# Performance work log

Hardware: AMD Instinct MI355X
Metric: run time of the kernel (lower is better)

Reference implementation:

```python
import jax, jax.numpy as jnp
import numpy as np

NUM_HEADS = 8
EPS = 1e-12  # torch F.normalize eps


def _l2norm(t):
    n = jnp.linalg.norm(t, axis=-1, keepdims=True)
    return t / jnp.maximum(n, EPS)


def setup_inputs() -> dict:
    key = jax.random.key(0)
    k1, k2, k3 = jax.random.split(key, 3)
    B, T, N, D = 16, 12, 1024, 128
    x = jax.random.normal(k1, (B, T, N, D), dtype=jnp.float32)
    # Linear(model_dim, 3*model_dim, bias=False): stored as (D, 3D) for x @ W
    W_qkv = jax.random.normal(k2, (D, 3 * D), dtype=jnp.float32) * (1.0 / np.sqrt(D))
    W_out = jax.random.normal(k3, (D, D), dtype=jnp.float32) * (1.0 / np.sqrt(D))
    b_out = jnp.zeros((D,), dtype=jnp.float32)
    return {"x": x, "W_qkv": W_qkv, "W_out": W_out, "b_out": b_out}


def reference(x, W_qkv, W_out, b_out):
    B, T, N, D = x.shape
    H = NUM_HEADS
    hd = D // H
    qkv = x @ W_qkv                                  # (B,T,N,3D)
    q, k, v = jnp.split(qkv, 3, axis=-1)
    # split heads + flatten (B,T) -> b = B*T, matching torch stack/flatten
    qs = _l2norm(q.reshape(B * T, N, H, hd))          # (b,N,H,m)
    ks = _l2norm(k.reshape(B * T, N, H, hd))
    vs = v.reshape(B * T, N, H, hd)
    # linear attention: running kv sum + normalizer
    kvs = jnp.einsum('blhm,blhd->bhmd', ks, vs)       # (b,H,m,d)
    attn_num = jnp.einsum('bnhm,bhmd->bnhd', qs, kvs) + N * vs
    ks_sum = jnp.sum(ks, axis=1)                      # (b,H,m)
    normalizer = jnp.einsum('bnhm,bhm->bnh', qs, ks_sum)[..., None] + N
    out = attn_num / normalizer                       # (b,N,H,d)
    out = out.reshape(B, T, N, D)
    return out @ W_out + b_out
```

## Files before the change

### kernel.cpp

```cpp
#include <hip/hip_runtime.h>

#define NBATCH 192
#define SEQ    1024
#define DIM    128
#define NH     8
#define EPS    1e-12f

typedef short bf16x8 __attribute__((ext_vector_type(8)));
typedef float f32x4  __attribute__((ext_vector_type(4)));

#define KVS_F  393216
#define ZERO_F 417792

static __device__ __forceinline__ unsigned short f2bf(float f) {
    unsigned u = __builtin_bit_cast(unsigned, f);
    u += 0x7fff + ((u >> 16) & 1);
    return (unsigned short)(u >> 16);
}

template <int CTRL>
static __device__ __forceinline__ float dpp_add(float v) {
    int j = __builtin_amdgcn_mov_dpp(__builtin_bit_cast(int, v), CTRL, 0xf, 0xf, false);
    return v + __builtin_bit_cast(float, j);
}
static __device__ __forceinline__ float r16sum(float v) {
    v = dpp_add<0xB1>(v);
    v = dpp_add<0x4E>(v);
    v = dpp_add<0x141>(v);
    v = dpp_add<0x140>(v);
    return v;
}

static __device__ __forceinline__ int strip_addr(int row, int el) {
    return row * 32 + ((((el >> 3) ^ (row & 3)) << 3) | (el & 7));
}

static __device__ __forceinline__ uint2 pack4(float a, float b, float c, float d) {
    uint2 r;
    r.x = (unsigned)f2bf(a) | ((unsigned)f2bf(b) << 16);
    r.y = (unsigned)f2bf(c) | ((unsigned)f2bf(d) << 16);
    return r;
}

static __device__ __forceinline__ bf16x8 cvt8(float4 a, float4 b) {
    bf16x8 r;
    r[0] = (short)f2bf(a.x); r[1] = (short)f2bf(a.y); r[2] = (short)f2bf(a.z); r[3] = (short)f2bf(a.w);
    r[4] = (short)f2bf(b.x); r[5] = (short)f2bf(b.y); r[6] = (short)f2bf(b.z); r[7] = (short)f2bf(b.w);
    return r;
}

static __device__ __forceinline__ bf16x8 gfrag(const unsigned short* __restrict__ wT,
                                               int ct, int ks, int lane) {
    return *reinterpret_cast<const bf16x8*>(wT + ((ct * 4 + ks) * 64 + lane) * 8);
}

__global__ __launch_bounds__(256) void k0_prep(const float* __restrict__ Wqkv,
                                               const float* __restrict__ Wout,
                                               unsigned short* __restrict__ wsWT) {
    int i = blockIdx.x * 256 + threadIdx.x;
    int which = i >> 14, e = i & 16383;
    int j = e & 7, f = e >> 3;
    int n15 = f & 15, q = (f >> 4) & 3, ks = (f >> 6) & 3, ct = f >> 8;
    int k = ks * 32 + q * 8 + j, n = ct * 16 + n15;
    float v = (which < 3) ? Wqkv[k * 384 + which * 128 + n] : Wout[k * 128 + n];
    wsWT[i] = f2bf(v);
}

__global__ __launch_bounds__(512, 4) void k1_kv(const float* __restrict__ x,
                                                const unsigned short* __restrict__ wsWT,
                                                float* __restrict__ kvs_ws,
                                                float* __restrict__ kssum_ws) {
    __shared__ float redf[16384];
    unsigned short* strips = reinterpret_cast<unsigned short*>(redf);
    int t = threadIdx.x, w = t >> 6, lane = t & 63, q = lane >> 4, n15 = lane & 15;
    int b = blockIdx.x >> 2, seg = blockIdx.x & 3;
    const unsigned short* wkT = wsWT + 16384;
    const unsigned short* wvT = wsWT + 32768;
    unsigned short* knS = strips + w * 1024;
    unsigned short* vS  = knS + 512;

    bf16x8 ah[2][4];
#pragma unroll
    for (int rs = 0; rs < 2; ++rs) {
        int row = seg * 256 + w * 32 + rs * 16 + n15;
        const float* xr = x + (size_t)(b * SEQ + row) * DIM;
#pragma unroll
        for (int ks = 0; ks < 4; ++ks) {
            float4 p0 = *reinterpret_cast<const float4*>(xr + ks * 32 + q * 8);
            float4 p1 = *reinterpret_cast<const float4*>(xr + ks * 32 + q * 8 + 4);
            ah[rs][ks] = cvt8(p0, p1);
        }
    }

    f32x4 kvsacc[8];
    float ksum[8];
#pragma unroll
    for (int h = 0; h < 8; ++h) { kvsacc[h] = (f32x4){0,0,0,0}; ksum[h] = 0.f; }

#pragma unroll
    for (int ct = 0; ct < 8; ++ct) {
        f32x4 ka[2] = {(f32x4){0,0,0,0}, (f32x4){0,0,0,0}};
        f32x4 va[2] = {(f32x4){0,0,0,0}, (f32x4){0,0,0,0}};
#pragma unroll
        for (int ks = 0; ks < 4; ++ks) {
            bf16x8 kb = gfrag(wkT, ct, ks, lane);
            bf16x8 vb = gfrag(wvT, ct, ks, lane);
#pragma unroll
            for (int rs = 0; rs < 2; ++rs) {
                ka[rs] = __builtin_amdgcn_mfma_f32_16x16x32_bf16(ah[rs][ks], kb, ka[rs], 0, 0, 0);
                va[rs] = __builtin_amdgcn_mfma_f32_16x16x32_bf16(ah[rs][ks], vb, va[rs], 0, 0, 0);
            }
        }
#pragma unroll
        for (int rs = 0; rs < 2; ++rs) {
            float kn[4];
#pragma unroll
            for (int r = 0; r < 4; ++r) {
                float val = ka[rs][r];
                float ssq = r16sum(val * val);
                float di  = 1.0f / fmaxf(sqrtf(ssq), EPS);
                kn[r] = val * di;
                ksum[ct] += kn[r];
            }
            *reinterpret_cast<uint2*>(knS + strip_addr(n15, rs * 16 + q * 4)) =
                pack4(kn[0], kn[1], kn[2], kn[3]);
            *reinterpret_cast<uint2*>(vS + strip_addr(n15, rs * 16 + q * 4)) =
                pack4(va[rs][0], va[rs][1], va[rs][2], va[rs][3]);
        }
        bf16x8 aK = *reinterpret_cast<const bf16x8*>(knS + strip_addr(n15, q * 8));
        bf16x8 bV = *reinterpret_cast<const bf16x8*>(vS + strip_addr(n15, q * 8));
        kvsacc[ct] = __builtin_amdgcn_mfma_f32_16x16x32_bf16(aK, bV, kvsacc[ct], 0, 0, 0);
    }

#pragma unroll
    for (int ct = 0; ct < 8; ++ct) {
        float s = ksum[ct];
        s += __shfl_xor(s, 16); s += __shfl_xor(s, 32);
        if (lane < 16) atomicAdd(&kssum_ws[b * 128 + ct * 16 + n15], s);
    }

    __syncthreads();
#pragma unroll
    for (int ct = 0; ct < 8; ++ct)
#pragma unroll
        for (int r = 0; r < 4; ++r)
            redf[w * 2048 + ct * 256 + (q * 4 + r) * 16 + n15] = kvsacc[ct][r];
    __syncthreads();
#pragma unroll
    for (int i = 0; i < 4; ++i) {
        int el = i * 512 + t;
        float s = 0.f;
#pragma unroll
        for (int ww = 0; ww < 8; ++ww) s += redf[ww * 2048 + el];
        atomicAdd(&kvs_ws[b * 2048 + el], s);
    }
}

__global__ __launch_bounds__(512, 4) void k2_out(const float* __restrict__ x,
                                                 const unsigned short* __restrict__ wsWT,
                                                 const float* __restrict__ kvs_ws,
                                                 const float* __restrict__ kssum_ws,
                                                 const float* __restrict__ bout,
                                                 float* __restrict__ out) {
    __shared__ unsigned short lds[40960];
    unsigned short* kvsT = lds;
    float* invS = reinterpret_cast<float*>(lds + 4096);
    unsigned short* tile = lds + 8192;
    int t = threadIdx.x, w = t >> 6, lane = t & 63, q = lane >> 4, n15 = lane & 15;
    int b = blockIdx.x >> 2, seg = blockIdx.x & 3, rowbase = seg * 256;
    const unsigned short* wqT = wsWT;
    const unsigned short* wvT = wsWT + 32768;
    const unsigned short* woT = wsWT + 49152;

    {
        int row = t >> 2, part = t & 3, h = row >> 4, d = row & 15;
        unsigned es[8];
#pragma unroll
        for (int j = 0; j < 8; j += 2) {
            int m0 = part * 8 + j;
            unsigned lo = (m0     < 16) ? f2bf(kvs_ws[b * 2048 + h * 256 + m0 * 16 + d])      : 0;
            unsigned hi = (m0 + 1 < 16) ? f2bf(kvs_ws[b * 2048 + h * 256 + (m0 + 1) * 16 + d]) : 0;
            es[j] = lo | (hi << 16);
        }
        uint4 v = {es[0], es[2], es[4], es[6]};
        *reinterpret_cast<uint4*>(kvsT + row * 32 + ((part ^ (row & 3)) << 3)) = v;
    }

    float kss[8];
#pragma unroll
    for (int h = 0; h < 8; ++h) kss[h] = kssum_ws[b * 128 + h * 16 + n15];

    bf16x8 ah[2][4];
#pragma unroll
    for (int rs = 0; rs < 2; ++rs) {
        int row = rowbase + w * 32 + rs * 16 + n15;
        const float* xr = x + (size_t)(b * SEQ + row) * DIM;
#pragma unroll
        for (int ks = 0; ks < 4; ++ks) {
            float4 p0 = *reinterpret_cast<const float4*>(xr + ks * 32 + q * 8);
            float4 p1 = *reinterpret_cast<const float4*>(xr + ks * 32 + q * 8 + 4);
            ah[rs][ks] = cvt8(p0, p1);
        }
    }

    unsigned short* tw   = tile + w * 4096;
    unsigned short* myS  = tw;
    float* myInv = invS + w * 256;
    {
        uint2 z = {0, 0};
        *reinterpret_cast<uint2*>(myS + strip_addr(n15, 16 + q * 4)) = z;
    }
    __syncthreads();

    f32x4 qacc[2][8];
#pragma unroll
    for (int rs = 0; rs < 2; ++rs)
#pragma unroll
        for (int h = 0; h < 8; ++h) qacc[rs][h] = (f32x4){0,0,0,0};
#pragma unroll
    for (int ct = 0; ct < 8; ++ct)
#pragma unroll
        for (int ks = 0; ks < 4; ++ks) {
            bf16x8 bb = gfrag(wqT, ct, ks, lane);
#pragma unroll
            for (int rs = 0; rs < 2; ++rs)
                qacc[rs][ct] = __builtin_amdgcn_mfma_f32_16x16x32_bf16(ah[rs][ks], bb, qacc[rs][ct], 0, 0, 0);
        }

    const float invSEQ = 1.0f / (float)SEQ;
    f32x4 nacc[2][8];
#pragma unroll
    for (int rs = 0; rs < 2; ++rs)
#pragma unroll
        for (int h = 0; h < 8; ++h) {
            float pv[4];
#pragma unroll
            for (int r = 0; r < 4; ++r) {
                float val = qacc[rs][h][r];
                float ssq = r16sum(val * val);
                float tt  = r16sum(val * kss[h]);
                float di  = 1.0f / fmaxf(sqrtf(ssq), EPS);
                float inv = 1.0f / (tt * di + (float)SEQ);
                pv[r] = val * di * invSEQ;
                if (n15 == 0) myInv[(rs * 16 + q * 4 + r) * 8 + h] = (float)SEQ * inv;
            }
#pragma unroll
            for (int r = 0; r < 4; ++r)
                myS[strip_addr(q * 4 + r, n15)] = f2bf(pv[r]);
            bf16x8 aq = *reinterpret_cast<const bf16x8*>(myS + strip_addr(n15, q * 8));
            bf16x8 bk = *reinterpret_cast<const bf16x8*>(kvsT + strip_addr(h * 16 + n15, q * 8));
            nacc[rs][h] = __builtin_amdgcn_mfma_f32_16x16x32_bf16(aq, bk, (f32x4){0,0,0,0}, 0, 0, 0);
        }

#pragma unroll
    for (int ct = 0; ct < 8; ++ct)
#pragma unroll
        for (int ks = 0; ks < 4; ++ks) {
            bf16x8 bb = gfrag(wvT, ct, ks, lane);
#pragma unroll
            for (int rs = 0; rs < 2; ++rs)
                nacc[rs][ct] = __builtin_amdgcn_mfma_f32_16x16x32_bf16(ah[rs][ks], bb, nacc[rs][ct], 0, 0, 0);
        }

#pragma unroll
    for (int rs = 0; rs < 2; ++rs)
#pragma unroll
        for (int h = 0; h < 8; ++h)
#pragma unroll
            for (int r = 0; r < 4; ++r) {
                float invN = myInv[(rs * 16 + q * 4 + r) * 8 + h];
                float pre  = nacc[rs][h][r] * invN;
                int rt = rs * 16 + q * 4 + r;
                int colg = h * 2 + (n15 >> 3);
                tw[rt * 128 + (((colg ^ (rt & 15)) << 3) | (n15 & 7))] = f2bf(pre);
            }

    bf16x8 ap[2][4];
#pragma unroll
    for (int rs = 0; rs < 2; ++rs)
#pragma unroll
        for (int ks = 0; ks < 4; ++ks) {
            int rt = rs * 16 + n15;
            ap[rs][ks] = *reinterpret_cast<const bf16x8*>(
                tw + rt * 128 + ((((ks << 2) + q) ^ (rt & 15)) << 3));
        }
    f32x4 oacc[2][8];
#pragma unroll
    for (int rs = 0; rs < 2; ++rs)
#pragma unroll
        for (int h = 0; h < 8; ++h) oacc[rs][h] = (f32x4){0,0,0,0};
#pragma unroll
    for (int ct = 0; ct < 8; ++ct)
#pragma unroll
        for (int ks = 0; ks < 4; ++ks) {
            bf16x8 bb = gfrag(woT, ct, ks, lane);
#pragma unroll
            for (int rs = 0; rs < 2; ++rs)
                oacc[rs][ct] = __builtin_amdgcn_mfma_f32_16x16x32_bf16(ap[rs][ks], bb, oacc[rs][ct], 0, 0, 0);
        }
#pragma unroll
    for (int ct = 0; ct < 8; ++ct) {
        float bo = bout[ct * 16 + n15];
#pragma unroll
        for (int rs = 0; rs < 2; ++rs)
#pragma unroll
            for (int r = 0; r < 4; ++r) {
                int row = rowbase + w * 32 + rs * 16 + q * 4 + r;
                out[(size_t)(b * SEQ + row) * DIM + ct * 16 + n15] = oacc[rs][ct][r] + bo;
            }
    }
}

extern "C" void kernel_launch(void* const* d_in, const int* in_sizes, int n_in,
                              void* d_out, int out_size, void* d_ws, size_t ws_size,
                              hipStream_t stream) {
    const float* x    = (const float*)d_in[0];
    const float* Wqkv = (const float*)d_in[1];
    const float* Wout = (const float*)d_in[2];
    const float* bout = (const float*)d_in[3];
    float* out = (float*)d_out;

    float* kvs_ws   = (float*)d_ws;
    float* kssum_ws = kvs_ws + KVS_F;
    unsigned short* wsWT = (unsigned short*)((char*)d_ws + (size_t)ZERO_F * 4);

    hipMemsetAsync(d_ws, 0, (size_t)ZERO_F * 4, stream);
    k0_prep<<<dim3(256), dim3(256), 0, stream>>>(Wqkv, Wout, wsWT);
    k1_kv<<<dim3(768), dim3(512), 0, stream>>>(x, wsWT, kvs_ws, kssum_ws);
    k2_out<<<dim3(768), dim3(512), 0, stream>>>(x, wsWT, kvs_ws, kssum_ws, bout, out);
}
```

Baseline: 329.2 us.

## Restructure k2 per row-strip: compute V then Q, fold normalizer into accumulator

```diff
diff --git a/kernel.cpp b/kernel.cpp
--- a/kernel.cpp
+++ b/kernel.cpp
@@ -163,9 +163,9 @@
                                                  const float* __restrict__ bout,
                                                  float* __restrict__ out) {
     __shared__ unsigned short lds[40960];
-    unsigned short* kvsT = lds;
-    float* invS = reinterpret_cast<float*>(lds + 4096);
-    unsigned short* tile = lds + 8192;
+    unsigned short* kvsT   = lds;
+    unsigned short* strips = lds + 4096;
+    unsigned short* tile   = lds + 8192;
     int t = threadIdx.x, w = t >> 6, lane = t & 63, q = lane >> 4, n15 = lane & 15;
     int b = blockIdx.x >> 2, seg = blockIdx.x & 3, rowbase = seg * 256;
     const unsigned short* wqT = wsWT;
@@ -203,77 +203,63 @@
         }
     }
 
-    unsigned short* tw   = tile + w * 4096;
-    unsigned short* myS  = tw;
-    float* myInv = invS + w * 256;
+    unsigned short* myS = strips + w * 512;
+    unsigned short* tw  = tile + w * 4096;
     {
         uint2 z = {0, 0};
         *reinterpret_cast<uint2*>(myS + strip_addr(n15, 16 + q * 4)) = z;
     }
     __syncthreads();
 
-    f32x4 qacc[2][8];
-#pragma unroll
-    for (int rs = 0; rs < 2; ++rs)
-#pragma unroll
-        for (int h = 0; h < 8; ++h) qacc[rs][h] = (f32x4){0,0,0,0};
-#pragma unroll
-    for (int ct = 0; ct < 8; ++ct)
-#pragma unroll
-        for (int ks = 0; ks < 4; ++ks) {
-            bf16x8 bb = gfrag(wqT, ct, ks, lane);
-#pragma unroll
-            for (int rs = 0; rs < 2; ++rs)
-                qacc[rs][ct] = __builtin_amdgcn_mfma_f32_16x16x32_bf16(ah[rs][ks], bb, qacc[rs][ct], 0, 0, 0);
-        }
-
-    const float invSEQ = 1.0f / (float)SEQ;
-    f32x4 nacc[2][8];
-#pragma unroll
-    for (int rs = 0; rs < 2; ++rs)
+#pragma unroll
+    for (int rs = 0; rs < 2; ++rs) {
+        f32x4 vacc[8];
+#pragma unroll
+        for (int h = 0; h < 8; ++h) vacc[h] = (f32x4){0,0,0,0};
+#pragma unroll
+        for (int ct = 0; ct < 8; ++ct)
+#pragma unroll
+            for (int ks = 0; ks < 4; ++ks) {
+                bf16x8 bb = gfrag(wvT, ct, ks, lane);
+                vacc[ct] = __builtin_amdgcn_mfma_f32_16x16x32_bf16(ah[rs][ks], bb, vacc[ct], 0, 0, 0);
+            }
+        f32x4 qacc[8];
+#pragma unroll
+        for (int h = 0; h < 8; ++h) qacc[h] = (f32x4){0,0,0,0};
+#pragma unroll
+        for (int ct = 0; ct < 8; ++ct)
+#pragma unroll
+            for (int ks = 0; ks < 4; ++ks) {
+                bf16x8 bb = gfrag(wqT, ct, ks, lane);
+                qacc[ct] = __builtin_amdgcn_mfma_f32_16x16x32_bf16(ah[rs][ks], bb, qacc[ct], 0, 0, 0);
+            }
 #pragma unroll
         for (int h = 0; h < 8; ++h) {
             float pv[4];
 #pragma unroll
             for (int r = 0; r < 4; ++r) {
-                float val = qacc[rs][h][r];
+                float val = qacc[h][r];
                 float ssq = r16sum(val * val);
                 float tt  = r16sum(val * kss[h]);
                 float di  = 1.0f / fmaxf(sqrtf(ssq), EPS);
                 float inv = 1.0f / (tt * di + (float)SEQ);
-                pv[r] = val * di * invSEQ;
-                if (n15 == 0) myInv[(rs * 16 + q * 4 + r) * 8 + h] = (float)SEQ * inv;
+                pv[r] = val * di * inv;
+                vacc[h][r] *= (float)SEQ * inv;
             }
 #pragma unroll
             for (int r = 0; r < 4; ++r)
                 myS[strip_addr(q * 4 + r, n15)] = f2bf(pv[r]);
             bf16x8 aq = *reinterpret_cast<const bf16x8*>(myS + strip_addr(n15, q * 8));
             bf16x8 bk = *reinterpret_cast<const bf16x8*>(kvsT + strip_addr(h * 16 + n15, q * 8));
-            nacc[rs][h] = __builtin_amdgcn_mfma_f32_16x16x32_bf16(aq, bk, (f32x4){0,0,0,0}, 0, 0, 0);
-        }
-
-#pragma unroll
-    for (int ct = 0; ct < 8; ++ct)
-#pragma unroll
-        for (int ks = 0; ks < 4; ++ks) {
-            bf16x8 bb = gfrag(wvT, ct, ks, lane);
-#pragma unroll
-            for (int rs = 0; rs < 2; ++rs)
-                nacc[rs][ct] = __builtin_amdgcn_mfma_f32_16x16x32_bf16(ah[rs][ks], bb, nacc[rs][ct], 0, 0, 0);
-        }
-
-#pragma unroll
-    for (int rs = 0; rs < 2; ++rs)
-#pragma unroll
-        for (int h = 0; h < 8; ++h)
+            vacc[h] = __builtin_amdgcn_mfma_f32_16x16x32_bf16(aq, bk, vacc[h], 0, 0, 0);
 #pragma unroll
             for (int r = 0; r < 4; ++r) {
-                float invN = myInv[(rs * 16 + q * 4 + r) * 8 + h];
-                float pre  = nacc[rs][h][r] * invN;
                 int rt = rs * 16 + q * 4 + r;
                 int colg = h * 2 + (n15 >> 3);
-                tw[rt * 128 + (((colg ^ (rt & 15)) << 3) | (n15 & 7))] = f2bf(pre);
-            }
+                tw[rt * 128 + (((colg ^ (rt & 15)) << 3) | (n15 & 7))] = f2bf(vacc[h][r]);
+            }
+        }
+    }
 
     bf16x8 ap[2][4];
 #pragma unroll
```

New measurement: 360.8 us. 1.1x slower.
